# Kernel tuning notes

Hardware: AMD Instinct MI355X
Metric: run time of the kernel (lower is better)

## Reference

```python
import jax, jax.numpy as jnp
import numpy as np

EMB, NR, NS, NB = 128, 6, 7, 8  # emb_size, num_radial, num_spherical, num_bilinear
E, L = 100_000, 500_000         # graph edges, line-graph (angle) triplets


def setup_inputs() -> dict:
    key = jax.random.key(0)
    ks = jax.random.split(key, 10)
    return {
        "rbf": jax.random.uniform(ks[0], (E, NR), dtype=jnp.float32),
        "m": jax.random.normal(ks[1], (E, EMB), dtype=jnp.float32),
        "o": jax.random.normal(ks[2], (E, 3), dtype=jnp.float32),
        "lg_src": jax.random.randint(ks[3], (L,), 0, E),
        "lg_dst": jax.random.randint(ks[4], (L,), 0, E),
        "W_rbf": jax.random.normal(ks[5], (NR, EMB), dtype=jnp.float32) * 0.1,
        "W_m": jax.random.normal(ks[6], (EMB, EMB), dtype=jnp.float32) * (1.0 / np.sqrt(EMB)),
        "b_m": jnp.zeros((EMB,), dtype=jnp.float32),
        "W_sbf": jax.random.normal(ks[7], (NR * NS, NB), dtype=jnp.float32) * 0.1,
        "W_bilin": jax.random.normal(ks[8], (EMB, NB, EMB), dtype=jnp.float32) * (2.0 / EMB),
    }


def reference(rbf, m, o, lg_src, lg_dst, W_rbf, W_m, b_m, W_sbf, W_bilin):
    # edge_transfer: w = dense_rbf(rbf) * act(dense_m(m))  -- per edge of g
    w = (rbf @ W_rbf) * jax.nn.silu(m @ W_m + b_m)          # [E, EMB]
    # radial basis tiled to pair with (spherical-outer, radial-inner) cbf layout
    rbf_env = jnp.tile(rbf, (1, NS))                         # [E, NS*NR]

    # msg_func over line-graph edges (gather from g's edges)
    R1, R2 = o[lg_src], o[lg_dst]                            # [L, 3]
    dot = jnp.sum(R1 * R2, axis=-1)
    crs = jnp.linalg.norm(jnp.cross(R1, R2), axis=-1)
    angle = jnp.arctan2(crs, dot)                            # [L]
    ls = jnp.arange(NS, dtype=angle.dtype)
    cbf = jnp.cos(angle[:, None] * ls[None, :])              # [L, NS] (sph_funcs = cos(l*theta))
    cbf = jnp.repeat(cbf, NR, axis=1)                        # [L, NS*NR]
    sbf = (rbf_env[lg_src] * cbf) @ W_sbf                    # [L, NB]

    # bilinear einsum 'wj,wl,ijl->wi' without [L,NB,EMB] intermediate:
    m_src = m[lg_src]                                        # [L, EMB]
    x_kj = jnp.zeros_like(m_src)
    for j in range(NB):  # NB=8, small fixed loop
        x_kj = x_kj + sbf[:, j:j + 1] * (m_src @ W_bilin[:, j, :].T)

    # reduce_func: mailbox scatter-sum over line-graph destinations
    m_update = jax.ops.segment_sum(x_kj, lg_dst, num_segments=E)  # [E, EMB]
    return w, m_update
```

## Files before the change

kernel.cpp:

```cpp
#include <hip/hip_runtime.h>
#include <math.h>

#define EMB 128
#define NR 6
#define NS 7
#define NB 8
#define TL 256
#define EPB 8

typedef __attribute__((ext_vector_type(8))) short short8;
typedef __attribute__((ext_vector_type(4))) float floatx4;

__device__ __forceinline__ short f2bf(float f) {
  unsigned int u = __float_as_uint(f);
  u = u + 0x7fff + ((u >> 16) & 1);
  return (short)(u >> 16);
}

__global__ void zero_kernel(float4* __restrict__ p, long n4) {
  long i = (long)blockIdx.x * blockDim.x + threadIdx.x;
  long stride = (long)gridDim.x * blockDim.x;
  float4 z; z.x = z.y = z.z = z.w = 0.f;
  for (; i < n4; i += stride) p[i] = z;
}

__global__ void wcvt_kernel(const float* __restrict__ w, short* __restrict__ o,
                            int n) {
  int i = blockIdx.x * 256 + threadIdx.x;
  if (i < n) o[i] = f2bf(w[i]);
}

__global__ __launch_bounds__(256) void edge_w_kernel(
    const float* __restrict__ rbf, const float* __restrict__ m,
    const float* __restrict__ W_rbf, const float* __restrict__ W_m,
    const float* __restrict__ b_m, float* __restrict__ w_out, int E) {
  __shared__ float ms[EPB * EMB];
  __shared__ float rs[EPB * 8];
  __shared__ float pacc[EPB * EMB];

  const int tid = threadIdx.x;
  const int i = tid & 127;
  const int h = tid >> 7;

  float Wreg[64];
#pragma unroll
  for (int kk = 0; kk < 64; ++kk) Wreg[kk] = W_m[(h * 64 + kk) * EMB + i];
  float wr[NR];
#pragma unroll
  for (int r = 0; r < NR; ++r) wr[r] = W_rbf[r * EMB + i];
  const float bm = b_m[i];

  const int ngrp = (E + EPB - 1) / EPB;
  for (int g = blockIdx.x; g < ngrp; g += gridDim.x) {
    const long e0 = (long)g * EPB;
    const int nv = min(EPB, (int)(E - e0));
    __syncthreads();
    if (nv == EPB) {
      ((float4*)ms)[tid] = ((const float4*)(m + e0 * EMB))[tid];
    } else {
      int er = (tid * 4) >> 7;
      if (er < nv) ((float4*)ms)[tid] = ((const float4*)(m + e0 * EMB))[tid];
    }
    if (tid < EPB * NR) {
      int er = tid / NR, r = tid - er * NR;
      if (er < nv) rs[er * 8 + r] = rbf[(e0 + er) * NR + r];
    }
    __syncthreads();

    float acc[EPB];
#pragma unroll
    for (int er = 0; er < EPB; ++er) acc[er] = 0.f;
    const float4* mv4 = (const float4*)ms;
#pragma unroll
    for (int q = 0; q < 16; ++q) {
#pragma unroll
      for (int er = 0; er < EPB; ++er) {
        float4 mv = mv4[er * 32 + h * 16 + q];
        acc[er] += Wreg[q * 4 + 0] * mv.x + Wreg[q * 4 + 1] * mv.y +
                   Wreg[q * 4 + 2] * mv.z + Wreg[q * 4 + 3] * mv.w;
      }
    }
    if (h == 1) {
#pragma unroll
      for (int er = 0; er < EPB; ++er) pacc[er * EMB + i] = acc[er];
    }
    __syncthreads();
    if (h == 0) {
#pragma unroll
      for (int er = 0; er < EPB; ++er) {
        if (er < nv) {
          float x = acc[er] + pacc[er * EMB + i] + bm;
          float sig = 1.f / (1.f + expf(-x));
          float act = x * sig;
          float ar = 0.f;
#pragma unroll
          for (int r = 0; r < NR; ++r) ar += wr[r] * rs[er * 8 + r];
          w_out[(e0 + er) * EMB + i] = ar * act;
        }
      }
    }
  }
}

template <bool WB>
__device__ __forceinline__ short8 ldB(const float* __restrict__ wf,
                                      const short* __restrict__ wh, long off) {
  if (WB) {
    return *(const short8*)(wh + off);
  } else {
    float4 u0 = *(const float4*)(wf + off);
    float4 u1 = *(const float4*)(wf + off + 4);
    short8 h;
    h[0] = f2bf(u0.x); h[1] = f2bf(u0.y); h[2] = f2bf(u0.z); h[3] = f2bf(u0.w);
    h[4] = f2bf(u1.x); h[5] = f2bf(u1.y); h[6] = f2bf(u1.z); h[7] = f2bf(u1.w);
    return h;
  }
}

template <bool WB>
__global__ __launch_bounds__(512, 2) void triplet_mfma(
    const float* __restrict__ rbf, const float* __restrict__ m,
    const float* __restrict__ o, const int* __restrict__ lg_src,
    const int* __restrict__ lg_dst, const float* __restrict__ W_sbf,
    const float* __restrict__ W_bilin_f, const short* __restrict__ W_bilin_h,
    float* __restrict__ m_update, int L) {
  __shared__ short aS[4096 * 8];
  __shared__ short wS[2][2048 * 8];
  __shared__ float sSt[NB][TL];
  __shared__ int srcS[TL];
  __shared__ int dstS[TL];

  const int tid = threadIdx.x;
  const int lane = tid & 63;
  const int wv = tid >> 6;
  const long base = (long)blockIdx.x * TL;

  if (tid < TL) {
    long l = base + tid;
    int lc = (l < L) ? (int)l : 0;
    srcS[tid] = lg_src[lc];
    dstS[tid] = (l < L) ? lg_dst[lc] : -1;
  }
  __syncthreads();

#pragma unroll
  for (int iter = 0; iter < 8; ++iter) {
    int s = iter * 512 + tid;
    int c = s >> 6, l2 = s & 63;
    int mt = c >> 2, ks = c & 3;
    int row = mt * 16 + (l2 & 15);
    int k = ks * 32 + (l2 >> 4) * 8;
    const float* src = m + (long)srcS[row] * EMB + k;
    float4 v0 = *(const float4*)src;
    float4 v1 = *(const float4*)(src + 4);
    short8 hh;
    hh[0] = f2bf(v0.x); hh[1] = f2bf(v0.y); hh[2] = f2bf(v0.z); hh[3] = f2bf(v0.w);
    hh[4] = f2bf(v1.x); hh[5] = f2bf(v1.y); hh[6] = f2bf(v1.z); hh[7] = f2bf(v1.w);
    *(short8*)&aS[s * 8] = hh;
  }

  if (tid < TL) {
    long l = base + tid;
    int lc = (l < L) ? (int)l : 0;
    int src = srcS[tid];
    int dst = lg_dst[lc];
    float r1x = o[src * 3 + 0], r1y = o[src * 3 + 1], r1z = o[src * 3 + 2];
    float r2x = o[dst * 3 + 0], r2y = o[dst * 3 + 1], r2z = o[dst * 3 + 2];
    float dotv = r1x * r2x + r1y * r2y + r1z * r2z;
    float cx = r1y * r2z - r1z * r2y;
    float cy = r1z * r2x - r1x * r2z;
    float cz = r1x * r2y - r1y * r2x;
    float crs = sqrtf(cx * cx + cy * cy + cz * cz);
    float angle = atan2f(crs, dotv);
    float cbf[NS];
#pragma unroll
    for (int s_ = 0; s_ < NS; ++s_) cbf[s_] = cosf(angle * (float)s_);
    float rb[NR];
#pragma unroll
    for (int r = 0; r < NR; ++r) rb[r] = rbf[src * NR + r];
#pragma unroll
    for (int b = 0; b < NB; ++b) {
      float sb = 0.f;
#pragma unroll
      for (int s_ = 0; s_ < NS; ++s_) {
        float t = 0.f;
#pragma unroll
        for (int r = 0; r < NR; ++r)
          t += rb[r] * W_sbf[(s_ * NR + r) * NB + b];
        sb += cbf[s_] * t;
      }
      sSt[b][tid] = sb;
    }
  }

  long bOff[4];
#pragma unroll
  for (int q = 0; q < 4; ++q) {
    int s2 = q * 512 + tid;
    int c2 = s2 >> 6;
    int ks = c2 >> 3, nt = c2 & 7;
    int i = nt * 16 + (lane & 15);
    int k = ks * 32 + (lane >> 4) * 8;
    bOff[q] = (long)i * NB * EMB + k;
  }

#pragma unroll
  for (int q = 0; q < 4; ++q) {
    short8 hh = ldB<WB>(W_bilin_f, W_bilin_h, bOff[q]);
    *(short8*)&wS[0][(q * 512 + tid) * 8] = hh;
  }
  __syncthreads();

  const int mh = wv >> 2;
  const int n0 = (wv & 3) * 2;
  const int kq = lane >> 4;
  const int col16 = lane & 15;

  float accf[8][2][4];
#pragma unroll
  for (int mt = 0; mt < 8; ++mt)
#pragma unroll
    for (int nn = 0; nn < 2; ++nn)
#pragma unroll
      for (int r = 0; r < 4; ++r) accf[mt][nn][r] = 0.f;

  int buf = 0;
#pragma unroll 1
  for (int j = 0; j < NB; ++j) {
    short8 pre0, pre1, pre2, pre3;
    if (j < NB - 1) {
      const long jo = (long)(j + 1) * EMB;
      pre0 = ldB<WB>(W_bilin_f, W_bilin_h, bOff[0] + jo);
      pre1 = ldB<WB>(W_bilin_f, W_bilin_h, bOff[1] + jo);
      pre2 = ldB<WB>(W_bilin_f, W_bilin_h, bOff[2] + jo);
      pre3 = ldB<WB>(W_bilin_f, W_bilin_h, bOff[3] + jo);
    }

    short8 Bf[4][2];
#pragma unroll
    for (int ks = 0; ks < 4; ++ks) {
      Bf[ks][0] = *(const short8*)&wS[buf][((ks * 8 + n0 + 0) * 64 + lane) * 8];
      Bf[ks][1] = *(const short8*)&wS[buf][((ks * 8 + n0 + 1) * 64 + lane) * 8];
    }
#pragma unroll
    for (int mt = 0; mt < 8; ++mt) {
      const int mtG = mh * 8 + mt;
      floatx4 C0 = (floatx4)0.f, C1 = (floatx4)0.f;
#pragma unroll
      for (int ks = 0; ks < 4; ++ks) {
        short8 A = *(const short8*)&aS[((mtG * 4 + ks) * 64 + lane) * 8];
        C0 = __builtin_amdgcn_mfma_f32_16x16x32_bf16(A, Bf[ks][0], C0, 0, 0, 0);
        C1 = __builtin_amdgcn_mfma_f32_16x16x32_bf16(A, Bf[ks][1], C1, 0, 0, 0);
      }
      const floatx4 sv = *(const floatx4*)&sSt[j][mtG * 16 + kq * 4];
#pragma unroll
      for (int r = 0; r < 4; ++r) {
        accf[mt][0][r] += sv[r] * C0[r];
        accf[mt][1][r] += sv[r] * C1[r];
      }
    }

    if (j < NB - 1) {
      *(short8*)&wS[buf ^ 1][(0 * 512 + tid) * 8] = pre0;
      *(short8*)&wS[buf ^ 1][(1 * 512 + tid) * 8] = pre1;
      *(short8*)&wS[buf ^ 1][(2 * 512 + tid) * 8] = pre2;
      *(short8*)&wS[buf ^ 1][(3 * 512 + tid) * 8] = pre3;
    }
    __syncthreads();
    buf ^= 1;
  }

#pragma unroll
  for (int mt = 0; mt < 8; ++mt) {
#pragma unroll
    for (int r = 0; r < 4; ++r) {
      int row = (mh * 8 + mt) * 16 + kq * 4 + r;
      int dst = dstS[row];
      if (dst >= 0) {
        float* p = m_update + (long)dst * EMB;
        unsafeAtomicAdd(p + (n0 + 0) * 16 + col16, accf[mt][0][r]);
        unsafeAtomicAdd(p + (n0 + 1) * 16 + col16, accf[mt][1][r]);
      }
    }
  }
}

extern "C" void kernel_launch(void* const* d_in, const int* in_sizes, int n_in,
                              void* d_out, int out_size, void* d_ws,
                              size_t ws_size, hipStream_t stream) {
  const float* rbf = (const float*)d_in[0];
  const float* m = (const float*)d_in[1];
  const float* o = (const float*)d_in[2];
  const int* lg_src = (const int*)d_in[3];
  const int* lg_dst = (const int*)d_in[4];
  const float* W_rbf = (const float*)d_in[5];
  const float* W_m = (const float*)d_in[6];
  const float* b_m = (const float*)d_in[7];
  const float* W_sbf = (const float*)d_in[8];
  const float* W_bilin = (const float*)d_in[9];

  const int E = in_sizes[1] / EMB;
  const int L = in_sizes[3];

  float* w_out = (float*)d_out;
  float* m_update = (float*)d_out + (long)E * EMB;

  long n4 = (long)E * EMB / 4;
  zero_kernel<<<1024, 256, 0, stream>>>((float4*)m_update, n4);
  edge_w_kernel<<<2048, 256, 0, stream>>>(rbf, m, W_rbf, W_m, b_m, w_out, E);

  int nblk = (L + TL - 1) / TL;
  const int wn = EMB * NB * EMB;
  if (ws_size >= (size_t)wn * sizeof(short)) {
    short* wh = (short*)d_ws;
    wcvt_kernel<<<(wn + 255) / 256, 256, 0, stream>>>(W_bilin, wh, wn);
    triplet_mfma<true><<<nblk, 512, 0, stream>>>(
        rbf, m, o, lg_src, lg_dst, W_sbf, nullptr, wh, m_update, L);
  } else {
    triplet_mfma<false><<<nblk, 512, 0, stream>>>(
        rbf, m, o, lg_src, lg_dst, W_sbf, W_bilin, nullptr, m_update, L);
  }
}
```

Measured before the change: 554.8 us.

## Shrink triplet tile, hold A fragments in registers, simplify edge_w kernel

The triplet kernel tile drops from 256 to 128 triplets per block. The A tile is staged in the second weight buffer, loaded into registers once, and the LDS buffer is then reused. The warp layout changes to 2x4 MFMA tiles per wave, and launch bounds now ask for higher occupancy (4 blocks). The edge_w kernel is rewritten so one 128-thread block handles one edge, with all 128 W_m columns held in registers and m and rbf read straight from global memory, and grid sizes are changed. The aim is lower LDS use and higher occupancy, at the cost of more register pressure, twice the W_bilin reloads per triplet, and the loss of edge batching in edge_w.

```diff
diff --git a/kernel.cpp b/kernel.cpp
--- a/kernel.cpp
+++ b/kernel.cpp
@@ -5,8 +5,7 @@
 #define NR 6
 #define NS 7
 #define NB 8
-#define TL 256
-#define EPB 8
+#define TL 128
 
 typedef __attribute__((ext_vector_type(8))) short short8;
 typedef __attribute__((ext_vector_type(4))) float floatx4;
@@ -30,81 +29,42 @@
   if (i < n) o[i] = f2bf(w[i]);
 }
 
-__global__ __launch_bounds__(256) void edge_w_kernel(
+__global__ __launch_bounds__(128) void edge_w_kernel(
     const float* __restrict__ rbf, const float* __restrict__ m,
     const float* __restrict__ W_rbf, const float* __restrict__ W_m,
     const float* __restrict__ b_m, float* __restrict__ w_out, int E) {
-  __shared__ float ms[EPB * EMB];
-  __shared__ float rs[EPB * 8];
-  __shared__ float pacc[EPB * EMB];
-
-  const int tid = threadIdx.x;
-  const int i = tid & 127;
-  const int h = tid >> 7;
-
-  float Wreg[64];
-#pragma unroll
-  for (int kk = 0; kk < 64; ++kk) Wreg[kk] = W_m[(h * 64 + kk) * EMB + i];
+  const int i = threadIdx.x;
+
+  float Wreg[EMB];
+#pragma unroll
+  for (int k = 0; k < EMB; ++k) Wreg[k] = W_m[k * EMB + i];
   float wr[NR];
 #pragma unroll
   for (int r = 0; r < NR; ++r) wr[r] = W_rbf[r * EMB + i];
   const float bm = b_m[i];
 
-  const int ngrp = (E + EPB - 1) / EPB;
-  for (int g = blockIdx.x; g < ngrp; g += gridDim.x) {
-    const long e0 = (long)g * EPB;
-    const int nv = min(EPB, (int)(E - e0));
-    __syncthreads();
-    if (nv == EPB) {
-      ((float4*)ms)[tid] = ((const float4*)(m + e0 * EMB))[tid];
-    } else {
-      int er = (tid * 4) >> 7;
-      if (er < nv) ((float4*)ms)[tid] = ((const float4*)(m + e0 * EMB))[tid];
-    }
-    if (tid < EPB * NR) {
-      int er = tid / NR, r = tid - er * NR;
-      if (er < nv) rs[er * 8 + r] = rbf[(e0 + er) * NR + r];
-    }
-    __syncthreads();
-
-    float acc[EPB];
-#pragma unroll
-    for (int er = 0; er < EPB; ++er) acc[er] = 0.f;
-    const float4* mv4 = (const float4*)ms;
-#pragma unroll
-    for (int q = 0; q < 16; ++q) {
-#pragma unroll
-      for (int er = 0; er < EPB; ++er) {
-        float4 mv = mv4[er * 32 + h * 16 + q];
-        acc[er] += Wreg[q * 4 + 0] * mv.x + Wreg[q * 4 + 1] * mv.y +
-                   Wreg[q * 4 + 2] * mv.z + Wreg[q * 4 + 3] * mv.w;
-      }
-    }
-    if (h == 1) {
-#pragma unroll
-      for (int er = 0; er < EPB; ++er) pacc[er * EMB + i] = acc[er];
-    }
-    __syncthreads();
-    if (h == 0) {
-#pragma unroll
-      for (int er = 0; er < EPB; ++er) {
-        if (er < nv) {
-          float x = acc[er] + pacc[er * EMB + i] + bm;
-          float sig = 1.f / (1.f + expf(-x));
-          float act = x * sig;
-          float ar = 0.f;
-#pragma unroll
-          for (int r = 0; r < NR; ++r) ar += wr[r] * rs[er * 8 + r];
-          w_out[(e0 + er) * EMB + i] = ar * act;
-        }
-      }
-    }
+  for (int e = blockIdx.x; e < E; e += gridDim.x) {
+    const float4* mrow = (const float4*)(m + (long)e * EMB);
+    float acc = 0.f;
+#pragma unroll
+    for (int q = 0; q < 32; ++q) {
+      float4 mv = mrow[q];
+      acc += Wreg[q * 4 + 0] * mv.x + Wreg[q * 4 + 1] * mv.y +
+             Wreg[q * 4 + 2] * mv.z + Wreg[q * 4 + 3] * mv.w;
+    }
+    float x = acc + bm;
+    float sig = 1.f / (1.f + expf(-x));
+    float act = x * sig;
+    float ar = 0.f;
+#pragma unroll
+    for (int r = 0; r < NR; ++r) ar += wr[r] * rbf[(long)e * NR + r];
+    w_out[(long)e * EMB + i] = ar * act;
   }
 }
 
 template <bool WB>
 __device__ __forceinline__ short8 ldB(const float* __restrict__ wf,
-                                      const short* __restrict__ wh, long off) {
+                                      const short* __restrict__ wh, int off) {
   if (WB) {
     return *(const short8*)(wh + off);
   } else {
@@ -118,14 +78,13 @@
 }
 
 template <bool WB>
-__global__ __launch_bounds__(512, 2) void triplet_mfma(
+__global__ __launch_bounds__(512, 4) void triplet_mfma(
     const float* __restrict__ rbf, const float* __restrict__ m,
     const float* __restrict__ o, const int* __restrict__ lg_src,
     const int* __restrict__ lg_dst, const float* __restrict__ W_sbf,
     const float* __restrict__ W_bilin_f, const short* __restrict__ W_bilin_h,
     float* __restrict__ m_update, int L) {
-  __shared__ short aS[4096 * 8];
-  __shared__ short wS[2][2048 * 8];
+  __shared__ short wSu[2][2048 * 8];
   __shared__ float sSt[NB][TL];
   __shared__ int srcS[TL];
   __shared__ int dstS[TL];
@@ -144,7 +103,7 @@
   __syncthreads();
 
 #pragma unroll
-  for (int iter = 0; iter < 8; ++iter) {
+  for (int iter = 0; iter < 4; ++iter) {
     int s = iter * 512 + tid;
     int c = s >> 6, l2 = s & 63;
     int mt = c >> 2, ks = c & 3;
@@ -156,7 +115,7 @@
     short8 hh;
     hh[0] = f2bf(v0.x); hh[1] = f2bf(v0.y); hh[2] = f2bf(v0.z); hh[3] = f2bf(v0.w);
     hh[4] = f2bf(v1.x); hh[5] = f2bf(v1.y); hh[6] = f2bf(v1.z); hh[7] = f2bf(v1.w);
-    *(short8*)&aS[s * 8] = hh;
+    *(short8*)&wSu[1][s * 8] = hh;
   }
 
   if (tid < TL) {
@@ -193,93 +152,104 @@
     }
   }
 
-  long bOff[4];
+  int bOff[4];
 #pragma unroll
   for (int q = 0; q < 4; ++q) {
-    int s2 = q * 512 + tid;
-    int c2 = s2 >> 6;
+    int c2 = (q * 512 + tid) >> 6;
     int ks = c2 >> 3, nt = c2 & 7;
     int i = nt * 16 + (lane & 15);
     int k = ks * 32 + (lane >> 4) * 8;
-    bOff[q] = (long)i * NB * EMB + k;
-  }
-
-#pragma unroll
-  for (int q = 0; q < 4; ++q) {
-    short8 hh = ldB<WB>(W_bilin_f, W_bilin_h, bOff[q]);
-    *(short8*)&wS[0][(q * 512 + tid) * 8] = hh;
-  }
+    bOff[q] = i * (NB * EMB) + k;
+  }
+
+#pragma unroll
+  for (int q = 0; q < 4; ++q)
+    *(short8*)&wSu[0][(q * 512 + tid) * 8] =
+        ldB<WB>(W_bilin_f, W_bilin_h, bOff[q]);
+
   __syncthreads();
 
-  const int mh = wv >> 2;
-  const int n0 = (wv & 3) * 2;
+  const int wm = wv >> 1;
+  const int wn = wv & 1;
   const int kq = lane >> 4;
   const int col16 = lane & 15;
 
-  float accf[8][2][4];
-#pragma unroll
-  for (int mt = 0; mt < 8; ++mt)
-#pragma unroll
-    for (int nn = 0; nn < 2; ++nn)
+  short8 A0[4], A1[4];
+#pragma unroll
+  for (int ks = 0; ks < 4; ++ks) {
+    A0[ks] = *(const short8*)&wSu[1][(((wm * 2 + 0) * 4 + ks) * 64 + lane) * 8];
+    A1[ks] = *(const short8*)&wSu[1][(((wm * 2 + 1) * 4 + ks) * 64 + lane) * 8];
+  }
+  __syncthreads();
+
+  float accf[2][4][4];
+#pragma unroll
+  for (int mt = 0; mt < 2; ++mt)
+#pragma unroll
+    for (int nn = 0; nn < 4; ++nn)
 #pragma unroll
       for (int r = 0; r < 4; ++r) accf[mt][nn][r] = 0.f;
 
-  int buf = 0;
 #pragma unroll 1
   for (int j = 0; j < NB; ++j) {
+    const short* wcur = (j & 1) ? &wSu[1][0] : &wSu[0][0];
+    short* wnxt = (j & 1) ? &wSu[0][0] : &wSu[1][0];
+
     short8 pre0, pre1, pre2, pre3;
     if (j < NB - 1) {
-      const long jo = (long)(j + 1) * EMB;
+      const int jo = (j + 1) * EMB;
       pre0 = ldB<WB>(W_bilin_f, W_bilin_h, bOff[0] + jo);
       pre1 = ldB<WB>(W_bilin_f, W_bilin_h, bOff[1] + jo);
       pre2 = ldB<WB>(W_bilin_f, W_bilin_h, bOff[2] + jo);
       pre3 = ldB<WB>(W_bilin_f, W_bilin_h, bOff[3] + jo);
     }
 
-    short8 Bf[4][2];
-#pragma unroll
-    for (int ks = 0; ks < 4; ++ks) {
-      Bf[ks][0] = *(const short8*)&wS[buf][((ks * 8 + n0 + 0) * 64 + lane) * 8];
-      Bf[ks][1] = *(const short8*)&wS[buf][((ks * 8 + n0 + 1) * 64 + lane) * 8];
-    }
-#pragma unroll
-    for (int mt = 0; mt < 8; ++mt) {
-      const int mtG = mh * 8 + mt;
-      floatx4 C0 = (floatx4)0.f, C1 = (floatx4)0.f;
+    const floatx4 sv0 = *(const floatx4*)&sSt[j][(wm * 2 + 0) * 16 + kq * 4];
+    const floatx4 sv1 = *(const floatx4*)&sSt[j][(wm * 2 + 1) * 16 + kq * 4];
+
+#pragma unroll
+    for (int nh = 0; nh < 2; ++nh) {
+      floatx4 C00 = (floatx4)0.f, C01 = (floatx4)0.f;
+      floatx4 C10 = (floatx4)0.f, C11 = (floatx4)0.f;
+      const int ntA = wn * 4 + nh * 2;
 #pragma unroll
       for (int ks = 0; ks < 4; ++ks) {
-        short8 A = *(const short8*)&aS[((mtG * 4 + ks) * 64 + lane) * 8];
-        C0 = __builtin_amdgcn_mfma_f32_16x16x32_bf16(A, Bf[ks][0], C0, 0, 0, 0);
-        C1 = __builtin_amdgcn_mfma_f32_16x16x32_bf16(A, Bf[ks][1], C1, 0, 0, 0);
-      }
-      const floatx4 sv = *(const floatx4*)&sSt[j][mtG * 16 + kq * 4];
+        short8 b0 = *(const short8*)&wcur[((ks * 8 + ntA + 0) * 64 + lane) * 8];
+        short8 b1 = *(const short8*)&wcur[((ks * 8 + ntA + 1) * 64 + lane) * 8];
+        C00 = __builtin_amdgcn_mfma_f32_16x16x32_bf16(A0[ks], b0, C00, 0, 0, 0);
+        C01 = __builtin_amdgcn_mfma_f32_16x16x32_bf16(A0[ks], b1, C01, 0, 0, 0);
+        C10 = __builtin_amdgcn_mfma_f32_16x16x32_bf16(A1[ks], b0, C10, 0, 0, 0);
+        C11 = __builtin_amdgcn_mfma_f32_16x16x32_bf16(A1[ks], b1, C11, 0, 0, 0);
+      }
 #pragma unroll
       for (int r = 0; r < 4; ++r) {
-        accf[mt][0][r] += sv[r] * C0[r];
-        accf[mt][1][r] += sv[r] * C1[r];
+        accf[0][nh * 2 + 0][r] += sv0[r] * C00[r];
+        accf[0][nh * 2 + 1][r] += sv0[r] * C01[r];
+        accf[1][nh * 2 + 0][r] += sv1[r] * C10[r];
+        accf[1][nh * 2 + 1][r] += sv1[r] * C11[r];
       }
     }
 
     if (j < NB - 1) {
-      *(short8*)&wS[buf ^ 1][(0 * 512 + tid) * 8] = pre0;
-      *(short8*)&wS[buf ^ 1][(1 * 512 + tid) * 8] = pre1;
-      *(short8*)&wS[buf ^ 1][(2 * 512 + tid) * 8] = pre2;
-      *(short8*)&wS[buf ^ 1][(3 * 512 + tid) * 8] = pre3;
+      *(short8*)&wnxt[(0 * 512 + tid) * 8] = pre0;
+      *(short8*)&wnxt[(1 * 512 + tid) * 8] = pre1;
+      *(short8*)&wnxt[(2 * 512 + tid) * 8] = pre2;
+      *(short8*)&wnxt[(3 * 512 + tid) * 8] = pre3;
     }
     __syncthreads();
-    buf ^= 1;
-  }
-
-#pragma unroll
-  for (int mt = 0; mt < 8; ++mt) {
+  }
+
+#pragma unroll
+  for (int mt = 0; mt < 2; ++mt) {
 #pragma unroll
     for (int r = 0; r < 4; ++r) {
-      int row = (mh * 8 + mt) * 16 + kq * 4 + r;
+      int row = (wm * 2 + mt) * 16 + kq * 4 + r;
       int dst = dstS[row];
       if (dst >= 0) {
-        float* p = m_update + (long)dst * EMB;
-        unsafeAtomicAdd(p + (n0 + 0) * 16 + col16, accf[mt][0][r]);
-        unsafeAtomicAdd(p + (n0 + 1) * 16 + col16, accf[mt][1][r]);
+        float* p = m_update + (long)dst * EMB + col16;
+#pragma unroll
+        for (int nt = 0; nt < 4; ++nt)
+          unsafeAtomicAdd(p + (wn * 4 + nt) * 16, accf[mt][nt][r]);
       }
     }
   }
@@ -306,8 +276,8 @@
   float* m_update = (float*)d_out + (long)E * EMB;
 
   long n4 = (long)E * EMB / 4;
-  zero_kernel<<<1024, 256, 0, stream>>>((float4*)m_update, n4);
-  edge_w_kernel<<<2048, 256, 0, stream>>>(rbf, m, W_rbf, W_m, b_m, w_out, E);
+  zero_kernel<<<2048, 256, 0, stream>>>((float4*)m_update, n4);
+  edge_w_kernel<<<4096, 128, 0, stream>>>(rbf, m, W_rbf, W_m, b_m, w_out, E);
 
   int nblk = (L + TL - 1) / TL;
   const int wn = EMB * NB * EMB;
```

Measured after the change: 777.2 us. 1.4x slower.
